# Kernel tuning notes

Hardware: AMD Instinct MI355X
Metric: run time of the kernel (lower is better)

Reference implementation:

```python
import jax, jax.numpy as jnp
import numpy as np

N = 4096
D_IMG = 512
D_FEAT = 512
D_H = 256
D_Z = 128
N_CLS = 64
CHANGE_FRAC = 1.0  # alpha


def setup_inputs() -> dict:
    key = jax.random.key(0)
    ks = jax.random.split(key, 12)
    u = jax.random.uniform(ks[0], (N, N))
    a = (jnp.triu(u, 1) < 0.01).astype(jnp.float32)
    adj_ori = a + a.T
    i = jnp.arange(N)
    # GCN-normalized adjacency D^-1/2 (A+I) D^-1/2 (input to ep_net)
    a_hat = adj_ori.at[i, i].set(1.0)
    d = jnp.power(a_hat.sum(1), -0.5)
    adj_norm = a_hat * d[:, None] * d[None, :]
    xav = lambda k, s: jax.random.uniform(k, s, jnp.float32, -1.0, 1.0) * jnp.sqrt(6.0 / (s[0] + s[1]))
    return {
        "adj_norm": adj_norm,
        "adj_ori": adj_ori,
        "feats_ori": jax.random.normal(ks[1], (N, D_FEAT), jnp.float32),
        "img_feats": jax.random.normal(ks[2], (N, D_IMG), jnp.float32),
        "csd_ori": jax.random.normal(ks[3], (N_CLS, D_FEAT), jnp.float32),
        "csd_img": jax.random.normal(ks[4], (N_CLS, D_IMG), jnp.float32),
        "noise": jax.random.normal(ks[5], (N, D_Z), jnp.float32),
        "Wb": xav(ks[6], (D_IMG, D_H)),
        "Wm": xav(ks[7], (D_H, D_Z)),
        "Wl": xav(ks[8], (D_H, D_Z)),
        "fc1_W": xav(ks[9], (2 * D_FEAT, D_H)),
        "fc1_b": jnp.zeros((D_H,), jnp.float32),
        "fc2_W": xav(ks[10], (2 * D_H, D_IMG)),
        "fc2_b": jnp.zeros((D_IMG,), jnp.float32),
    }


def _ceil_st(x):
    # CeilNoGradient: ceil forward, identity backward (straight-through)
    return x + jax.lax.stop_gradient(jnp.ceil(x) - x)


def _gsage_layer(adj, h, W, b, relu):
    neigh = adj @ h
    mean_neigh = neigh / (adj.sum(axis=1, keepdims=True) + 1e-7)
    x = jnp.concatenate((h, mean_neigh), axis=1) @ W + b
    return jax.nn.relu(x) if relu else x


def _sample_adj_edge(adj_logits, adj):
    n_edges = jnp.sum(adj != 0)
    n_change = jnp.floor(n_edges.astype(jnp.float32) * CHANGE_FRAC / 2.0).astype(jnp.int32)
    ep = jnp.triu(adj_logits, 1)
    ep = ep - jnp.min(ep)
    ep = ep / jnp.max(ep)
    T = N * N
    # --- remove lowest-prob existing edges ---
    mask_rm = ep * adj
    v = jnp.sort(mask_rm.reshape(-1))  # ascending; positives at the tail
    n_nz = jnp.sum(v > 0)
    n_rm = jnp.minimum(n_nz, n_change)
    thresh_rm = v[T - n_nz + n_rm - 1]  # n_rm-th smallest positive
    mask_rm = jnp.where(mask_rm > thresh_rm, 0.0, mask_rm)
    mask_rm = _ceil_st(mask_rm)
    mask_rm = mask_rm + mask_rm.T
    adj_new = adj - mask_rm
    # --- add highest-prob missing edges ---
    mask_add = ep * (1.0 - adj)
    v2 = jnp.sort(mask_add.reshape(-1))
    n_nz2 = jnp.sum(v2 > 0)
    n_add = jnp.minimum(n_nz2, n_change)
    thresh_add = v2[T - n_add]  # n_add-th largest positive
    mask_add = jnp.where(mask_add < thresh_add, 0.0, mask_add)
    mask_add = _ceil_st(mask_add)
    mask_add = mask_add + mask_add.T
    return adj_new + mask_add


def reference(adj_norm, adj_ori, feats_ori, img_feats, csd_ori, csd_img, noise,
              Wb, Wm, Wl, fc1_W, fc1_b, fc2_W, fc2_b):
    # ep_net (VGAE, gae=False)
    hidden = adj_norm @ (img_feats @ Wb)
    mean = jax.nn.relu(adj_norm @ (hidden @ Wm))
    logstd = jax.nn.relu(adj_norm @ (hidden @ Wl))
    Z = noise * jnp.exp(logstd) + mean
    adj_logits = Z @ Z.T
    # edge rewiring
    adj_new = _sample_adj_edge(adj_logits, adj_ori)
    # normalize_adj for 'gsage': fill diag 1, L1 row-normalize
    i = jnp.arange(N)
    adj_new = adj_new.at[i, i].set(1.0)
    adj_new = adj_new / jnp.maximum(jnp.sum(jnp.abs(adj_new), axis=1, keepdims=True), 1e-12)
    # nc_net (DGPN)
    preds_img = img_feats @ csd_img.T
    h1 = _gsage_layer(adj_new, feats_ori, fc1_W, fc1_b, relu=True)
    h2 = _gsage_layer(adj_new, h1, fc2_W, fc2_b, relu=False)
    feat_total = jax.nn.log_softmax(h2, axis=-1)
    preds_total = feat_total @ csd_img.T
    return preds_total, feat_total, preds_img, adj_logits
```

## Files before the change

### kernel.cpp

```cpp
#include <hip/hip_runtime.h>
#include <type_traits>
#include <stdint.h>

#define NN 4096
#define TTOT 16777216UL

enum { F_RELU=1, F_ACC=2, F_RS=4, F_BIAS=8 };

typedef unsigned short ushort_t;
using bf16x8 = __attribute__((ext_vector_type(8))) short;
using f32x4  = __attribute__((ext_vector_type(4))) float;

struct SelParams {
  unsigned min_ord, max_ord, n_up;
  float lo, M, c0;
  unsigned n_change, rm_prefix, rm_k, add_prefix, add_k;
  float t_rm, t_add;
  unsigned hist_rm[256], hist_add[256];
};

__device__ __forceinline__ unsigned ordenc(float x){
  unsigned u = __float_as_uint(x);
  return (u & 0x80000000u) ? ~u : (u | 0x80000000u);
}
__device__ __forceinline__ float orddec_ok(unsigned o){
  unsigned u = (o & 0x80000000u) ? (o ^ 0x80000000u) : ~o;
  return __uint_as_float(u);
}
__device__ __forceinline__ ushort_t f2bf(float x){
  unsigned u = __float_as_uint(x);
  return (ushort_t)((u + 0x7FFFu + ((u >> 16) & 1u)) >> 16);
}
__device__ __forceinline__ float bf2f(ushort_t h){
  return __uint_as_float(((unsigned)h) << 16);
}

template<int DN>
__global__ __launch_bounds__(256)
void k_b3t(const float* __restrict__ Bsrc, ushort_t* __restrict__ H,
           ushort_t* __restrict__ Mg, ushort_t* __restrict__ L)
{
  __shared__ ushort_t sh[64][65], sm[64][65], sl[64][65];
  const int t = threadIdx.x;
  const int n0 = blockIdx.x * 64, k0 = blockIdx.y * 64;
  #pragma unroll
  for (int it = 0; it < 16; ++it){
    int idx = it*256 + t; int r = idx >> 6, c = idx & 63;
    float x  = Bsrc[(size_t)(k0 + r)*DN + n0 + c];
    ushort_t hb = f2bf(x);
    float r1 = x - bf2f(hb);
    ushort_t mb = f2bf(r1);
    float r2 = r1 - bf2f(mb);
    ushort_t lb = f2bf(r2);
    sh[r][c] = hb; sm[r][c] = mb; sl[r][c] = lb;
  }
  __syncthreads();
  #pragma unroll
  for (int it = 0; it < 16; ++it){
    int idx = it*256 + t; int r = idx >> 6, c = idx & 63;
    size_t o = (size_t)(n0 + r)*4096 + k0 + c;
    H[o] = sh[c][r]; Mg[o] = sm[c][r]; L[o] = sl[c][r];
  }
}

__global__ __launch_bounds__(256)
void k_mfma(const signed char* __restrict__ A8,
            const ushort_t* __restrict__ BH, const ushort_t* __restrict__ BM2,
            const ushort_t* __restrict__ BL, float* __restrict__ C, int N)
{
  __shared__ ushort_t Ab[64][72];
  __shared__ ushort_t Bb[3][64][72];
  const int t = threadIdx.x;
  const int m0 = blockIdx.y * 64, n0 = blockIdx.x * 64;
  const int sr = t >> 2, sc = (t & 3) * 16;
  const int w = t >> 6, lane = t & 63;
  const int fr = lane & 15, fg = lane >> 4;

  int4 a_r = *reinterpret_cast<const int4*>(A8 + (size_t)(m0+sr)*4096 + sc);
  const ushort_t* bsrc0 = BH  + (size_t)(n0+sr)*4096 + sc;
  const ushort_t* bsrc1 = BM2 + (size_t)(n0+sr)*4096 + sc;
  const ushort_t* bsrc2 = BL  + (size_t)(n0+sr)*4096 + sc;
  int4 b0a = reinterpret_cast<const int4*>(bsrc0)[0], b0b = reinterpret_cast<const int4*>(bsrc0)[1];
  int4 b1a = reinterpret_cast<const int4*>(bsrc1)[0], b1b = reinterpret_cast<const int4*>(bsrc1)[1];
  int4 b2a = reinterpret_cast<const int4*>(bsrc2)[0], b2b = reinterpret_cast<const int4*>(bsrc2)[1];

  f32x4 acc[4][3];
  #pragma unroll
  for (int c = 0; c < 4; ++c)
    #pragma unroll
    for (int p = 0; p < 3; ++p)
      acc[c][p] = (f32x4){0.f, 0.f, 0.f, 0.f};

  for (int k0 = 0; k0 < 4096; k0 += 64){
    {
      alignas(16) ushort_t tmp[16];
      const signed char* ab = reinterpret_cast<const signed char*>(&a_r);
      #pragma unroll
      for (int i = 0; i < 16; ++i) tmp[i] = f2bf((float)(int)ab[i]);
      *reinterpret_cast<int4*>(&Ab[sr][sc])     = reinterpret_cast<int4*>(tmp)[0];
      *reinterpret_cast<int4*>(&Ab[sr][sc + 8]) = reinterpret_cast<int4*>(tmp)[1];
      *reinterpret_cast<int4*>(&Bb[0][sr][sc])     = b0a;
      *reinterpret_cast<int4*>(&Bb[0][sr][sc + 8]) = b0b;
      *reinterpret_cast<int4*>(&Bb[1][sr][sc])     = b1a;
      *reinterpret_cast<int4*>(&Bb[1][sr][sc + 8]) = b1b;
      *reinterpret_cast<int4*>(&Bb[2][sr][sc])     = b2a;
      *reinterpret_cast<int4*>(&Bb[2][sr][sc + 8]) = b2b;
    }
    __syncthreads();
    if (k0 + 64 < 4096){
      a_r = *reinterpret_cast<const int4*>(A8 + (size_t)(m0+sr)*4096 + (k0+64) + sc);
      const ushort_t* p0 = BH  + (size_t)(n0+sr)*4096 + (k0+64) + sc;
      const ushort_t* p1 = BM2 + (size_t)(n0+sr)*4096 + (k0+64) + sc;
      const ushort_t* p2 = BL  + (size_t)(n0+sr)*4096 + (k0+64) + sc;
      b0a = reinterpret_cast<const int4*>(p0)[0]; b0b = reinterpret_cast<const int4*>(p0)[1];
      b1a = reinterpret_cast<const int4*>(p1)[0]; b1b = reinterpret_cast<const int4*>(p1)[1];
      b2a = reinterpret_cast<const int4*>(p2)[0]; b2b = reinterpret_cast<const int4*>(p2)[1];
    }
    #pragma unroll
    for (int kk = 0; kk < 64; kk += 32){
      bf16x8 af = *reinterpret_cast<const bf16x8*>(&Ab[w*16 + fr][kk + fg*8]);
      #pragma unroll
      for (int c = 0; c < 4; ++c){
        const int bn = c*16 + fr;
        bf16x8 bh = *reinterpret_cast<const bf16x8*>(&Bb[0][bn][kk + fg*8]);
        acc[c][0] = __builtin_amdgcn_mfma_f32_16x16x32_bf16(af, bh, acc[c][0], 0, 0, 0);
        bf16x8 bm = *reinterpret_cast<const bf16x8*>(&Bb[1][bn][kk + fg*8]);
        acc[c][1] = __builtin_amdgcn_mfma_f32_16x16x32_bf16(af, bm, acc[c][1], 0, 0, 0);
        bf16x8 bl = *reinterpret_cast<const bf16x8*>(&Bb[2][bn][kk + fg*8]);
        acc[c][2] = __builtin_amdgcn_mfma_f32_16x16x32_bf16(af, bl, acc[c][2], 0, 0, 0);
      }
    }
    __syncthreads();
  }
  #pragma unroll
  for (int c = 0; c < 4; ++c){
    f32x4 s = acc[c][0] + acc[c][1];
    s = s + acc[c][2];
    #pragma unroll
    for (int r = 0; r < 4; ++r)
      C[(size_t)(m0 + w*16 + fg*4 + r)*N + n0 + c*16 + fr] = s[r];
  }
}

template<typename TA>
__global__ __launch_bounds__(256)
void k_gemm32(const TA* __restrict__ A, const float* __restrict__ B,
              float* __restrict__ C, int M, int N, int K, int ldc,
              const float* __restrict__ rowscale, const float* __restrict__ bias,
              int flags)
{
  __shared__ float As[16][36];
  __shared__ float Bs[16][68];
  const int t  = threadIdx.x;
  const int tx = t & 15, ty = t >> 4;
  const int m0 = blockIdx.y * 32, n0 = blockIdx.x * 64;
  float acc[2][4] = {};
  for (int k0 = 0; k0 < K; k0 += 16) {
    if (t < 128){
      const int mA = t >> 2, kA = (t & 3) * 4;
      if constexpr (std::is_same<TA, float>::value) {
        float4 v = *reinterpret_cast<const float4*>(A + (size_t)(m0+mA)*K + (k0+kA));
        As[kA+0][mA]=v.x; As[kA+1][mA]=v.y; As[kA+2][mA]=v.z; As[kA+3][mA]=v.w;
      } else {
        int u = *reinterpret_cast<const int*>(A + (size_t)(m0+mA)*K + (k0+kA));
        As[kA+0][mA]=(float)(int)(signed char)( u       & 0xff);
        As[kA+1][mA]=(float)(int)(signed char)((u>>8)   & 0xff);
        As[kA+2][mA]=(float)(int)(signed char)((u>>16)  & 0xff);
        As[kA+3][mA]=(float)(int)(signed char)((u>>24)  & 0xff);
      }
    }
    {
      const int kB = t >> 4, nB = (t & 15) * 4;
      float4 w = *reinterpret_cast<const float4*>(B + (size_t)(k0+kB)*N + (n0+nB));
      Bs[kB][nB+0]=w.x; Bs[kB][nB+1]=w.y; Bs[kB][nB+2]=w.z; Bs[kB][nB+3]=w.w;
    }
    __syncthreads();
    #pragma unroll
    for (int kk = 0; kk < 16; ++kk) {
      float a0 = As[kk][ty*2+0];
      float a1 = As[kk][ty*2+1];
      float4 bv = *reinterpret_cast<const float4*>(&Bs[kk][tx*4]);
      float b[4]={bv.x,bv.y,bv.z,bv.w};
      #pragma unroll
      for (int j=0;j<4;++j){
        acc[0][j] = fmaf(a0, b[j], acc[0][j]);
        acc[1][j] = fmaf(a1, b[j], acc[1][j]);
      }
    }
    __syncthreads();
  }
  #pragma unroll
  for (int i=0;i<2;++i){
    const int m = m0 + ty*2 + i;
    const float rsv = (flags & F_RS) ? rowscale[m] : 1.0f;
    float* cp = C + (size_t)m*ldc + (n0 + tx*4);
    float o[4];
    #pragma unroll
    for (int j=0;j<4;++j){
      float v = acc[i][j] * rsv;
      if (flags & F_BIAS) v += bias[n0 + tx*4 + j];
      if (flags & F_ACC)  v += cp[j];
      if (flags & F_RELU) v = fmaxf(v, 0.0f);
      o[j] = v;
    }
    *reinterpret_cast<float4*>(cp) = make_float4(o[0],o[1],o[2],o[3]);
  }
}

__global__ __launch_bounds__(256)
void k_gemm32T(const float* __restrict__ A, const float* __restrict__ B,
               float* __restrict__ C, int M, int N, int K, int ldc)
{
  __shared__ float As[16][36];
  __shared__ float Bs[16][68];
  const int t  = threadIdx.x;
  const int tx = t & 15, ty = t >> 4;
  const int m0 = blockIdx.y * 32, n0 = blockIdx.x * 64;
  float acc[2][4] = {};
  for (int k0 = 0; k0 < K; k0 += 16) {
    if (t < 128){
      const int mA = t >> 2, kA = (t & 3) * 4;
      float4 v = *reinterpret_cast<const float4*>(A + (size_t)(m0+mA)*K + (k0+kA));
      As[kA+0][mA]=v.x; As[kA+1][mA]=v.y; As[kA+2][mA]=v.z; As[kA+3][mA]=v.w;
    }
    {
      const int nB = t >> 2, kB = (t & 3) * 4;
      float4 w = *reinterpret_cast<const float4*>(B + (size_t)(n0+nB)*K + (k0+kB));
      Bs[kB+0][nB]=w.x; Bs[kB+1][nB]=w.y; Bs[kB+2][nB]=w.z; Bs[kB+3][nB]=w.w;
    }
    __syncthreads();
    #pragma unroll
    for (int kk = 0; kk < 16; ++kk) {
      float a0 = As[kk][ty*2+0];
      float a1 = As[kk][ty*2+1];
      float4 bv = *reinterpret_cast<const float4*>(&Bs[kk][tx*4]);
      float b[4]={bv.x,bv.y,bv.z,bv.w};
      #pragma unroll
      for (int j=0;j<4;++j){
        acc[0][j] = fmaf(a0, b[j], acc[0][j]);
        acc[1][j] = fmaf(a1, b[j], acc[1][j]);
      }
    }
    __syncthreads();
  }
  #pragma unroll
  for (int i=0;i<2;++i){
    const int m = m0 + ty*2 + i;
    float* cp = C + (size_t)m*ldc + (n0 + tx*4);
    *reinterpret_cast<float4*>(cp) = make_float4(acc[i][0],acc[i][1],acc[i][2],acc[i][3]);
  }
}

__global__ __launch_bounds__(256)
void k_fc(const float* __restrict__ A1, const float* __restrict__ B1,
          const float* __restrict__ bias,
          const float* __restrict__ A2, const float* __restrict__ B2,
          const float* __restrict__ rowscale,
          float* __restrict__ C, int N, int K1, int K2, int relu)
{
  __shared__ float As[16][36];
  __shared__ float Bs[16][68];
  const int t  = threadIdx.x;
  const int tx = t & 15, ty = t >> 4;
  const int m0 = blockIdx.y * 32, n0 = blockIdx.x * 64;
  float acc1[2][4] = {};
  float acc2[2][4] = {};
  for (int k0 = 0; k0 < K1; k0 += 16) {
    if (t < 128){
      const int mA = t >> 2, kA = (t & 3) * 4;
      float4 v = *reinterpret_cast<const float4*>(A1 + (size_t)(m0+mA)*K1 + (k0+kA));
      As[kA+0][mA]=v.x; As[kA+1][mA]=v.y; As[kA+2][mA]=v.z; As[kA+3][mA]=v.w;
    }
    {
      const int kB = t >> 4, nB = (t & 15) * 4;
      float4 w = *reinterpret_cast<const float4*>(B1 + (size_t)(k0+kB)*N + (n0+nB));
      Bs[kB][nB+0]=w.x; Bs[kB][nB+1]=w.y; Bs[kB][nB+2]=w.z; Bs[kB][nB+3]=w.w;
    }
    __syncthreads();
    #pragma unroll
    for (int kk = 0; kk < 16; ++kk) {
      float a0 = As[kk][ty*2+0];
      float a1 = As[kk][ty*2+1];
      float4 bv = *reinterpret_cast<const float4*>(&Bs[kk][tx*4]);
      float b[4]={bv.x,bv.y,bv.z,bv.w};
      #pragma unroll
      for (int j=0;j<4;++j){
        acc1[0][j] = fmaf(a0, b[j], acc1[0][j]);
        acc1[1][j] = fmaf(a1, b[j], acc1[1][j]);
      }
    }
    __syncthreads();
  }
  for (int k0 = 0; k0 < K2; k0 += 16) {
    if (t < 128){
      const int mA = t >> 2, kA = (t & 3) * 4;
      float4 v = *reinterpret_cast<const float4*>(A2 + (size_t)(m0+mA)*K2 + (k0+kA));
      As[kA+0][mA]=v.x; As[kA+1][mA]=v.y; As[kA+2][mA]=v.z; As[kA+3][mA]=v.w;
    }
    {
      const int kB = t >> 4, nB = (t & 15) * 4;
      float4 w = *reinterpret_cast<const float4*>(B2 + (size_t)(k0+kB)*N + (n0+nB));
      Bs[kB][nB+0]=w.x; Bs[kB][nB+1]=w.y; Bs[kB][nB+2]=w.z; Bs[kB][nB+3]=w.w;
    }
    __syncthreads();
    #pragma unroll
    for (int kk = 0; kk < 16; ++kk) {
      float a0 = As[kk][ty*2+0];
      float a1 = As[kk][ty*2+1];
      float4 bv = *reinterpret_cast<const float4*>(&Bs[kk][tx*4]);
      float b[4]={bv.x,bv.y,bv.z,bv.w};
      #pragma unroll
      for (int j=0;j<4;++j){
        acc2[0][j] = fmaf(a0, b[j], acc2[0][j]);
        acc2[1][j] = fmaf(a1, b[j], acc2[1][j]);
      }
    }
    __syncthreads();
  }
  #pragma unroll
  for (int i=0;i<2;++i){
    const int m = m0 + ty*2 + i;
    const float rsv = rowscale[m];
    float* cp = C + (size_t)m*N + (n0 + tx*4);
    float o[4];
    #pragma unroll
    for (int j=0;j<4;++j){
      float t1 = acc1[i][j] + bias[n0 + tx*4 + j];
      float v  = acc2[i][j] * rsv;
      v += t1;
      if (relu) v = fmaxf(v, 0.0f);
      o[j] = v;
    }
    *reinterpret_cast<float4*>(cp) = make_float4(o[0],o[1],o[2],o[3]);
  }
}

__global__ __launch_bounds__(256)
void k_wcat(const float* __restrict__ Wm, const float* __restrict__ Wl,
            float* __restrict__ Wcat)
{
  int idx = blockIdx.x*256 + threadIdx.x;
  int row = idx >> 8, col = idx & 255;
  Wcat[idx] = (col < 128) ? Wm[row*128 + col] : Wl[row*128 + (col - 128)];
}

template<int D>
__global__ __launch_bounds__(256)
void k_spmmF(const float* __restrict__ A, const float* __restrict__ B,
             float* __restrict__ C)
{
  const int row = blockIdx.x, t = threadIdx.x;
  const int lane = t & 63, wv = t >> 6;
  __shared__ int   sc[288];
  __shared__ float sv[288];
  __shared__ int wtot[4];
  __shared__ int nsh;
  const float4* r4 = reinterpret_cast<const float4*>(A + (size_t)row*NN) + t*4;
  float lv[16];
  #pragma unroll
  for (int q=0;q<4;++q){
    float4 v = r4[q];
    lv[q*4+0]=v.x; lv[q*4+1]=v.y; lv[q*4+2]=v.z; lv[q*4+3]=v.w;
  }
  int c = 0;
  #pragma unroll
  for (int k=0;k<16;++k) c += (lv[k] != 0.0f);
  int inc = c;
  #pragma unroll
  for (int off=1; off<64; off<<=1){
    int v = __shfl_up(inc, off, 64);
    if (lane >= off) inc += v;
  }
  if (lane == 63) wtot[wv] = inc;
  __syncthreads();
  int wbase = 0;
  #pragma unroll
  for (int ww=0; ww<3; ++ww) if (ww < wv) wbase += wtot[ww];
  int pos = wbase + inc - c;
  #pragma unroll
  for (int k=0;k<16;++k){
    if (lv[k] != 0.0f){
      if (pos >= 0 && pos < 288){ sc[pos] = t*16+k; sv[pos] = lv[k]; }
      pos++;
    }
  }
  if (t == 255){
    int tot = wbase + inc;
    nsh = (tot < 288) ? tot : 288;
  }
  __syncthreads();
  const int n = nsh;
  float acc = 0.f;
  int s = 0;
  for (; s+4 <= n; s += 4){
    float x0 = B[(size_t)sc[s+0]*D + t];
    float x1 = B[(size_t)sc[s+1]*D + t];
    float x2 = B[(size_t)sc[s+2]*D + t];
    float x3 = B[(size_t)sc[s+3]*D + t];
    acc = fmaf(sv[s+0], x0, acc);
    acc = fmaf(sv[s+1], x1, acc);
    acc = fmaf(sv[s+2], x2, acc);
    acc = fmaf(sv[s+3], x3, acc);
  }
  for (; s < n; ++s) acc = fmaf(sv[s], B[(size_t)sc[s]*D + t], acc);
  C[(size_t)row*D + t] = acc;
}

__global__ __launch_bounds__(256)
void k_zzt(const float* __restrict__ Z, float* __restrict__ C)
{
  const int bx = blockIdx.x, by = blockIdx.y;
  if (by > bx) return;
  __shared__ float As[16][68];
  __shared__ float Bs[16][68];
  const int t = threadIdx.x, tx = t & 15, ty = t >> 4;
  const int m0 = by*64, n0 = bx*64;
  const int mA = t >> 2, kA = (t & 3) * 4;
  float acc[4][4] = {};
  for (int k0 = 0; k0 < 128; k0 += 16){
    float4 va = *reinterpret_cast<const float4*>(Z + (size_t)(m0+mA)*128 + k0 + kA);
    As[kA+0][mA]=va.x; As[kA+1][mA]=va.y; As[kA+2][mA]=va.z; As[kA+3][mA]=va.w;
    float4 vb = *reinterpret_cast<const float4*>(Z + (size_t)(n0+mA)*128 + k0 + kA);
    Bs[kA+0][mA]=vb.x; Bs[kA+1][mA]=vb.y; Bs[kA+2][mA]=vb.z; Bs[kA+3][mA]=vb.w;
    __syncthreads();
    #pragma unroll
    for (int kk = 0; kk < 16; ++kk) {
      float4 av = *reinterpret_cast<const float4*>(&As[kk][ty*4]);
      float4 bv = *reinterpret_cast<const float4*>(&Bs[kk][tx*4]);
      float a[4]={av.x,av.y,av.z,av.w};
      float b[4]={bv.x,bv.y,bv.z,bv.w};
      #pragma unroll
      for (int i=0;i<4;++i)
        #pragma unroll
        for (int j=0;j<4;++j)
          acc[i][j] = fmaf(a[i], b[j], acc[i][j]);
    }
    __syncthreads();
  }
  #pragma unroll
  for (int i=0;i<4;++i){
    float* cp = C + (size_t)(m0+ty*4+i)*NN + (n0 + tx*4);
    *reinterpret_cast<float4*>(cp) = make_float4(acc[i][0],acc[i][1],acc[i][2],acc[i][3]);
  }
  if (bx != by){
    for (int c0 = 0; c0 < 64; c0 += 16){
      __syncthreads();
      if (tx >= c0/4 && tx < c0/4 + 4){
        #pragma unroll
        for (int i=0;i<4;++i)
          #pragma unroll
          for (int j=0;j<4;++j)
            As[tx*4 + j - c0][ty*4 + i] = acc[i][j];
      }
      __syncthreads();
      const int c = t & 63, r0 = t >> 6;
      #pragma unroll
      for (int rr = 0; rr < 4; ++rr)
        C[(size_t)(n0 + c0 + r0 + rr*4)*NN + m0 + c] = As[r0 + rr*4][c];
    }
  }
}

__global__ __launch_bounds__(256)
void k_z2(const float* __restrict__ MPLP, const float* __restrict__ noise,
          float* __restrict__ Z)
{
  int i = blockIdx.x*256 + threadIdx.x;
  int m = i >> 7, c = i & 127;
  float mp = fmaxf(MPLP[(size_t)m*256 + c], 0.0f);
  float lp = fmaxf(MPLP[(size_t)m*256 + 128 + c], 0.0f);
  Z[i] = noise[i]*expf(lp) + mp;
}

__global__ __launch_bounds__(256)
void k_initstats(SelParams* p)
{
  int t = threadIdx.x;
  if (t == 0){
    p->min_ord = 0xFFFFFFFFu; p->max_ord = 0u; p->n_up = 0u;
    p->rm_prefix = 0u; p->add_prefix = 0u;
  }
  p->hist_rm[t] = 0u; p->hist_add[t] = 0u;
}

__global__ __launch_bounds__(256)
void k_stats1(const float* __restrict__ L, const float* __restrict__ adj,
              unsigned long long* __restrict__ mask, SelParams* __restrict__ p)
{
  unsigned mn=0xFFFFFFFFu, mx=0u, cnt=0u;
  size_t g = (size_t)blockIdx.x*256 + threadIdx.x;
  const size_t stride = (size_t)gridDim.x*256;
  for (; g < 262144; g += stride){
    const int i  = (int)(g >> 6);
    const int jb = (int)(g & 63) << 6;
    unsigned long long m = 0ull;
    if (jb + 63 > i){
      const float4* a4 = reinterpret_cast<const float4*>(adj + (size_t)i*NN + jb);
      const float4* l4 = reinterpret_cast<const float4*>(L   + (size_t)i*NN + jb);
      for (int w = 0; w < 16; ++w){
        const int j0 = jb + w*4;
        if (j0 + 3 <= i) continue;
        float4 av = a4[w]; float4 lv = l4[w];
        float ae[4]={av.x,av.y,av.z,av.w};
        float le[4]={lv.x,lv.y,lv.z,lv.w};
        #pragma unroll
        for (int e=0;e<4;++e){
          const int jj = j0 + e;
          if (jj > i){
            if (ae[e] != 0.0f){ m |= 1ull << (jj & 63); cnt++; }
            unsigned o = ordenc(le[e]);
            mn = (o < mn) ? o : mn;
            mx = (o > mx) ? o : mx;
          }
        }
      }
    }
    mask[g] = m;
  }
  __shared__ unsigned smn[256], smx[256], sc[256];
  int t = threadIdx.x;
  smn[t]=mn; smx[t]=mx; sc[t]=cnt; __syncthreads();
  for (int s=128; s>0; s>>=1){
    if (t < s){
      smn[t] = (smn[t+s] < smn[t]) ? smn[t+s] : smn[t];
      smx[t] = (smx[t+s] > smx[t]) ? smx[t+s] : smx[t];
      sc[t] += sc[t+s];
    }
    __syncthreads();
  }
  if (t == 0){
    atomicMin(&p->min_ord, smn[0]);
    atomicMax(&p->max_ord, smx[0]);
    atomicAdd(&p->n_up, sc[0]);
  }
}

__global__ void k_stats2(SelParams* p)
{
  float mnv = orddec_ok(p->min_ord), mxv = orddec_ok(p->max_ord);
  float lo = fminf(mnv, 0.0f), hi = fmaxf(mxv, 0.0f);
  p->lo = lo;
  p->M  = hi - lo;
  p->c0 = (0.0f - lo) / p->M;
  p->n_change = p->n_up;
}

__global__ __launch_bounds__(256)
void k_hist2(const float* __restrict__ L, const unsigned long long* __restrict__ mask,
             SelParams* __restrict__ p, int shift)
{
  __shared__ unsigned hr[256], ha[256];
  const int t = threadIdx.x;
  hr[t]=0u; ha[t]=0u; __syncthreads();
  const float lo = p->lo, Mv = p->M;
  const unsigned pr = p->rm_prefix, pa = p->add_prefix;
  const float4* L4 = reinterpret_cast<const float4*>(L);
  size_t q = (size_t)blockIdx.x*256 + t;
  const size_t stride = (size_t)gridDim.x*256;
  for (; q < TTOT/4; q += stride){
    const int i = (int)(q >> 10);
    const int j = (int)(q & 1023) << 2;
    if (j + 3 <= i) continue;
    float4 l = L4[q];
    const unsigned long long w = mask[q >> 4];
    float le[4]={l.x,l.y,l.z,l.w};
    #pragma unroll
    for (int e=0;e<4;++e){
      const int jj = j + e;
      if (jj <= i) continue;
      const unsigned key = __float_as_uint((le[e] - lo) / Mv);
      if (key == 0u) continue;
      const bool edge = (w >> (jj & 63)) & 1ull;
      if (edge){
        if (shift == 24 || (key >> (shift+8)) == pr) atomicAdd(&hr[(key>>shift)&255u], 1u);
      } else {
        if (shift == 24 || (key >> (shift+8)) == pa) atomicAdd(&ha[(key>>shift)&255u], 1u);
      }
    }
  }
  __syncthreads();
  if (hr[t]) atomicAdd(&p->hist_rm[t], hr[t]);
  if (ha[t]) atomicAdd(&p->hist_add[t], ha[t]);
}

__global__ __launch_bounds__(256)
void k_scan2(SelParams* __restrict__ p, int shift)
{
  const int t = threadIdx.x;
  if (t == 0){
    const unsigned c0k  = __float_as_uint(p->c0);
    const unsigned n_up = p->n_up;
    {
      unsigned injb = 300u, inj = 0u;
      if (c0k != 0u && (shift == 24 || (c0k >> (shift+8)) == p->rm_prefix)){
        injb = (c0k >> shift) & 255u; inj = n_up;
      }
      unsigned k;
      if (shift == 24){
        unsigned tot = inj;
        for (int d=0; d<256; ++d) tot += p->hist_rm[d];
        k = (tot < p->n_change) ? tot : p->n_change;
      } else k = p->rm_k;
      unsigned cum = 0u, digit = 255u;
      for (int d=0; d<256; ++d){
        unsigned hd = p->hist_rm[d] + (((unsigned)d == injb) ? inj : 0u);
        if (cum + hd >= k){ digit = (unsigned)d; k -= cum; break; }
        cum += hd;
      }
      p->rm_prefix = (p->rm_prefix << 8) | digit;
      p->rm_k = k;
      if (shift == 0) p->t_rm = __uint_as_float(p->rm_prefix);
    }
    {
      unsigned injb = 300u, inj = 0u;
      if (c0k != 0u && (shift == 24 || (c0k >> (shift+8)) == p->add_prefix)){
        injb = (c0k >> shift) & 255u;
        inj  = 8386560u - n_up + 4096u;
      }
      unsigned k;
      if (shift == 24){
        unsigned tot = inj;
        for (int d=0; d<256; ++d) tot += p->hist_add[d];
        k = (tot < p->n_change) ? tot : p->n_change;
      } else k = p->add_k;
      unsigned cum = 0u, digit = 0u;
      for (int d=255; d>=0; --d){
        unsigned hd = p->hist_add[d] + (((unsigned)d == injb) ? inj : 0u);
        if (cum + hd >= k){ digit = (unsigned)d; k -= cum; break; }
        cum += hd;
      }
      p->add_prefix = (p->add_prefix << 8) | digit;
      p->add_k = k;
      if (shift == 0) p->t_add = __uint_as_float(p->add_prefix);
    }
  }
  __syncthreads();
  p->hist_rm[t] = 0u; p->hist_add[t] = 0u;
}

__device__ __forceinline__ int adjval(bool edge, float v, float c0v, float trm, float tad)
{
  int rmU = (edge && v   >  0.0f && v   <= trm) ? 1 : 0;
  int rmL = (edge && c0v >  0.0f && c0v <= trm) ? 1 : 0;
  int adU = (!edge && v   >= tad) ? 1 : 0;
  int adL = (!edge && c0v >= tad) ? 1 : 0;
  return (edge ? 1 : 0) - rmU - rmL + adU + adL;
}

__global__ __launch_bounds__(256)
void k_apply(const float* __restrict__ L, const unsigned long long* __restrict__ mask,
             const SelParams* __restrict__ p, signed char* __restrict__ A8)
{
  const int bx = blockIdx.x, by = blockIdx.y;
  if (by > bx) return;
  const float lo=p->lo, Mv=p->M, c0v=p->c0, trm=p->t_rm, tad=p->t_add;
  const int i0 = by*64, j0 = bx*64, t = threadIdx.x;
  __shared__ signed char Vs[64][65];
  if (bx == by){
    for (int it=0; it<16; ++it){
      int e = it*256 + t; int r = e>>6, c = e&63;
      size_t idx = (size_t)(i0+r)*NN + (j0+c);
      if (r < c){
        bool edge = (mask[idx>>6] >> ((j0+c) & 63)) & 1ull;
        float v = (L[idx] - lo) / Mv;
        int val = adjval(edge, v, c0v, trm, tad);
        A8[idx] = (signed char)val;
        Vs[c][r] = (signed char)val;
      } else if (r == c){
        A8[idx] = 1;
      }
    }
    __syncthreads();
    for (int it=0; it<16; ++it){
      int e = it*256 + t; int r = e>>6, c = e&63;
      if (r > c) A8[(size_t)(i0+r)*NN + (j0+c)] = Vs[r][c];
    }
  } else {
    for (int it=0; it<16; ++it){
      int e = it*256 + t; int r = e>>6, c = e&63;
      size_t idx = (size_t)(i0+r)*NN + (j0+c);
      bool edge = (mask[idx>>6] >> ((j0+c) & 63)) & 1ull;
      float v = (L[idx] - lo) / Mv;
      int val = adjval(edge, v, c0v, trm, tad);
      A8[idx] = (signed char)val;
      Vs[c][r] = (signed char)val;
    }
    __syncthreads();
    for (int it=0; it<16; ++it){
      int e = it*256 + t; int r = e>>6, c = e&63;
      A8[(size_t)(j0+r)*NN + (i0+c)] = Vs[r][c];
    }
  }
}

__global__ __launch_bounds__(256)
void k_rowsum8(const signed char* __restrict__ A8, float* __restrict__ s_mean)
{
  const int row = blockIdx.x, t = threadIdx.x;
  const int4 w = reinterpret_cast<const int4*>(A8 + (size_t)row*NN)[t];
  int s = 0, a = 0;
  int vs[4] = {w.x, w.y, w.z, w.w};
  #pragma unroll
  for (int q=0; q<4; ++q){
    int u = vs[q];
    #pragma unroll
    for (int b=0; b<4; ++b){
      int c = (int)(signed char)((u >> (8*b)) & 0xff);
      s += c; a += (c < 0) ? -c : c;
    }
  }
  __shared__ int rs_[256], ra_[256];
  rs_[t]=s; ra_[t]=a; __syncthreads();
  for (int st=128; st>0; st>>=1){
    if (t < st){ rs_[t]+=rs_[t+st]; ra_[t]+=ra_[t+st]; }
    __syncthreads();
  }
  if (t == 0){
    float rs = (float)rs_[0], ra = (float)ra_[0];
    float A = fmaxf(ra, 1e-12f);
    s_mean[row] = (1.0f / A) / (rs / A + 1e-7f);
  }
}

__global__ __launch_bounds__(256)
void k_lsm(float* __restrict__ X)
{
  const int row = blockIdx.x, t = threadIdx.x;
  float* x = X + (size_t)row*512;
  float v0 = x[t], v1 = x[t+256];
  __shared__ float red[256];
  red[t] = fmaxf(v0, v1); __syncthreads();
  for (int s=128; s>0; s>>=1){
    if (t < s) red[t] = fmaxf(red[t], red[t+s]);
    __syncthreads();
  }
  float m = red[0]; __syncthreads();
  red[t] = expf(v0-m) + expf(v1-m); __syncthreads();
  for (int s=128; s>0; s>>=1){
    if (t < s) red[t] += red[t+s];
    __syncthreads();
  }
  float ls = logf(red[0]);
  x[t]     = (v0 - m) - ls;
  x[t+256] = (v1 - m) - ls;
}

extern "C" void kernel_launch(void* const* d_in, const int* in_sizes, int n_in,
                              void* d_out, int out_size, void* d_ws, size_t ws_size,
                              hipStream_t stream)
{
  (void)in_sizes; (void)n_in; (void)out_size; (void)ws_size;
  const float* adj_norm = (const float*)d_in[0];
  const float* adj_ori  = (const float*)d_in[1];
  const float* feats    = (const float*)d_in[2];
  const float* img      = (const float*)d_in[3];
  const float* csd_img  = (const float*)d_in[5];
  const float* noise    = (const float*)d_in[6];
  const float* Wb       = (const float*)d_in[7];
  const float* Wm       = (const float*)d_in[8];
  const float* Wl       = (const float*)d_in[9];
  const float* fc1W     = (const float*)d_in[10];
  const float* fc1b     = (const float*)d_in[11];
  const float* fc2W     = (const float*)d_in[12];
  const float* fc2b     = (const float*)d_in[13];

  float* out    = (float*)d_out;
  float* out_pt = out;
  float* out_ft = out + 262144;
  float* out_pi = out + 2359296;
  float* out_lg = out + 2621440;

  char* W = (char*)d_ws;
  signed char* adj8 = (signed char*)W;
  float* bufA   = (float*)(W + (16u<<20));
  float* bufB   = (float*)(W + (24u<<20));
  float* HMHL   = (float*)(W + (28u<<20));
  float* MPLP   = (float*)(W + (32u<<20));
  float* Z      = (float*)(W + (36u<<20));
  unsigned long long* mask = (unsigned long long*)(W + (38u<<20));
  float* s_mean = (float*)(W + (44u<<20));
  SelParams* sp = (SelParams*)(W + (44u<<20) + 65536);
  float* Wcat   = (float*)(W + (45u<<20));
  ushort_t* BT1h = (ushort_t*)(W + (28u<<20));
  ushort_t* BT1m = (ushort_t*)(W + (32u<<20));
  ushort_t* BT1l = (ushort_t*)(W + (36u<<20));
  ushort_t* BT2h = (ushort_t*)(W + (28u<<20));
  ushort_t* BT2m = (ushort_t*)(W + (30u<<20));
  ushort_t* BT2l = (ushort_t*)(W + (32u<<20));

  dim3 B(256);
  auto G32 = [](int M, int N){ return dim3((unsigned)(N/64), (unsigned)(M/32)); };

  k_gemm32<float><<<G32(4096,256),B,0,stream>>>(img, Wb, bufA, 4096,256,512,256, nullptr,nullptr,0);
  k_spmmF<256><<<4096,B,0,stream>>>(adj_norm, bufA, bufB);
  k_wcat<<<256,B,0,stream>>>(Wm, Wl, Wcat);
  k_gemm32<float><<<G32(4096,256),B,0,stream>>>(bufB, Wcat, HMHL, 4096,256,256,256, nullptr,nullptr,0);
  k_spmmF<256><<<4096,B,0,stream>>>(adj_norm, HMHL, MPLP);
  k_z2<<<2048,B,0,stream>>>(MPLP, noise, Z);
  k_zzt<<<dim3(64,64),B,0,stream>>>(Z, out_lg);

  k_initstats<<<1,B,0,stream>>>(sp);
  k_stats1<<<1024,B,0,stream>>>(out_lg, adj_ori, mask, sp);
  k_stats2<<<1,1,0,stream>>>(sp);
  for (int shift = 24; shift >= 0; shift -= 8){
    k_hist2<<<2048,B,0,stream>>>(out_lg, mask, sp, shift);
    k_scan2<<<1,B,0,stream>>>(sp, shift);
  }
  k_apply<<<dim3(64,64),B,0,stream>>>(out_lg, mask, sp, adj8);

  k_rowsum8<<<4096,B,0,stream>>>(adj8, s_mean);

  k_b3t<512><<<dim3(8,64),B,0,stream>>>(feats, BT1h, BT1m, BT1l);
  k_mfma<<<dim3(8,64),B,0,stream>>>(adj8, BT1h, BT1m, BT1l, bufA, 512);
  k_fc<<<G32(4096,256),B,0,stream>>>(feats, fc1W, fc1b, bufA, fc1W + 512*256, s_mean,
                                     bufB, 256, 512, 512, 1);
  k_b3t<256><<<dim3(4,64),B,0,stream>>>(bufB, BT2h, BT2m, BT2l);
  k_mfma<<<dim3(4,64),B,0,stream>>>(adj8, BT2h, BT2m, BT2l, bufA, 256);
  k_fc<<<G32(4096,512),B,0,stream>>>(bufB, fc2W, fc2b, bufA, fc2W + 256*512, s_mean,
                                     out_ft, 512, 256, 256, 0);
  k_lsm<<<4096,B,0,stream>>>(out_ft);

  k_gemm32T<<<G32(4096,64),B,0,stream>>>(out_ft, csd_img, out_pt, 4096,64,512,64);
  k_gemm32T<<<G32(4096,64),B,0,stream>>>(img, csd_img, out_pi, 4096,64,512,64);
}
```

Measured before the change: 855.4 us.

## Load B operand fragments straight from global memory, dropping B shared-memory staging

The three-way split-bf16 MFMA GEMM kernel no longer stages the B (hi/mid/lo) tiles through LDS. Each wave now owns a 16-column strip of B and loads its fragments directly from global into registers, while iterating over the four 16-row A tiles from LDS. This removes LDS traffic and the store/load for B, but the B global loads are no longer prefetched a tile ahead, so their latency may be exposed inside the MFMA loop.

```diff
diff --git a/kernel.cpp b/kernel.cpp
--- a/kernel.cpp
+++ b/kernel.cpp
@@ -69,27 +69,24 @@
             const ushort_t* __restrict__ BL, float* __restrict__ C, int N)
 {
   __shared__ ushort_t Ab[64][72];
-  __shared__ ushort_t Bb[3][64][72];
   const int t = threadIdx.x;
   const int m0 = blockIdx.y * 64, n0 = blockIdx.x * 64;
   const int sr = t >> 2, sc = (t & 3) * 16;
   const int w = t >> 6, lane = t & 63;
   const int fr = lane & 15, fg = lane >> 4;
+  const size_t brow = (size_t)(n0 + w*16 + fr) * 4096 + (size_t)(fg*8);
+  const ushort_t* bh = BH  + brow;
+  const ushort_t* bm = BM2 + brow;
+  const ushort_t* bl = BL  + brow;
 
   int4 a_r = *reinterpret_cast<const int4*>(A8 + (size_t)(m0+sr)*4096 + sc);
-  const ushort_t* bsrc0 = BH  + (size_t)(n0+sr)*4096 + sc;
-  const ushort_t* bsrc1 = BM2 + (size_t)(n0+sr)*4096 + sc;
-  const ushort_t* bsrc2 = BL  + (size_t)(n0+sr)*4096 + sc;
-  int4 b0a = reinterpret_cast<const int4*>(bsrc0)[0], b0b = reinterpret_cast<const int4*>(bsrc0)[1];
-  int4 b1a = reinterpret_cast<const int4*>(bsrc1)[0], b1b = reinterpret_cast<const int4*>(bsrc1)[1];
-  int4 b2a = reinterpret_cast<const int4*>(bsrc2)[0], b2b = reinterpret_cast<const int4*>(bsrc2)[1];
 
   f32x4 acc[4][3];
   #pragma unroll
-  for (int c = 0; c < 4; ++c)
+  for (int mt = 0; mt < 4; ++mt)
     #pragma unroll
     for (int p = 0; p < 3; ++p)
-      acc[c][p] = (f32x4){0.f, 0.f, 0.f, 0.f};
+      acc[mt][p] = (f32x4){0.f, 0.f, 0.f, 0.f};
 
   for (int k0 = 0; k0 < 4096; k0 += 64){
     {
@@ -99,46 +96,32 @@
       for (int i = 0; i < 16; ++i) tmp[i] = f2bf((float)(int)ab[i]);
       *reinterpret_cast<int4*>(&Ab[sr][sc])     = reinterpret_cast<int4*>(tmp)[0];
       *reinterpret_cast<int4*>(&Ab[sr][sc + 8]) = reinterpret_cast<int4*>(tmp)[1];
-      *reinterpret_cast<int4*>(&Bb[0][sr][sc])     = b0a;
-      *reinterpret_cast<int4*>(&Bb[0][sr][sc + 8]) = b0b;
-      *reinterpret_cast<int4*>(&Bb[1][sr][sc])     = b1a;
-      *reinterpret_cast<int4*>(&Bb[1][sr][sc + 8]) = b1b;
-      *reinterpret_cast<int4*>(&Bb[2][sr][sc])     = b2a;
-      *reinterpret_cast<int4*>(&Bb[2][sr][sc + 8]) = b2b;
-    }
-    __syncthreads();
-    if (k0 + 64 < 4096){
+    }
+    __syncthreads();
+    if (k0 + 64 < 4096)
       a_r = *reinterpret_cast<const int4*>(A8 + (size_t)(m0+sr)*4096 + (k0+64) + sc);
-      const ushort_t* p0 = BH  + (size_t)(n0+sr)*4096 + (k0+64) + sc;
-      const ushort_t* p1 = BM2 + (size_t)(n0+sr)*4096 + (k0+64) + sc;
-      const ushort_t* p2 = BL  + (size_t)(n0+sr)*4096 + (k0+64) + sc;
-      b0a = reinterpret_cast<const int4*>(p0)[0]; b0b = reinterpret_cast<const int4*>(p0)[1];
-      b1a = reinterpret_cast<const int4*>(p1)[0]; b1b = reinterpret_cast<const int4*>(p1)[1];
-      b2a = reinterpret_cast<const int4*>(p2)[0]; b2b = reinterpret_cast<const int4*>(p2)[1];
-    }
     #pragma unroll
     for (int kk = 0; kk < 64; kk += 32){
-      bf16x8 af = *reinterpret_cast<const bf16x8*>(&Ab[w*16 + fr][kk + fg*8]);
+      bf16x8 b0 = *reinterpret_cast<const bf16x8*>(bh + k0 + kk);
+      bf16x8 b1 = *reinterpret_cast<const bf16x8*>(bm + k0 + kk);
+      bf16x8 b2 = *reinterpret_cast<const bf16x8*>(bl + k0 + kk);
       #pragma unroll
-      for (int c = 0; c < 4; ++c){
-        const int bn = c*16 + fr;
-        bf16x8 bh = *reinterpret_cast<const bf16x8*>(&Bb[0][bn][kk + fg*8]);
-        acc[c][0] = __builtin_amdgcn_mfma_f32_16x16x32_bf16(af, bh, acc[c][0], 0, 0, 0);
-        bf16x8 bm = *reinterpret_cast<const bf16x8*>(&Bb[1][bn][kk + fg*8]);
-        acc[c][1] = __builtin_amdgcn_mfma_f32_16x16x32_bf16(af, bm, acc[c][1], 0, 0, 0);
-        bf16x8 bl = *reinterpret_cast<const bf16x8*>(&Bb[2][bn][kk + fg*8]);
-        acc[c][2] = __builtin_amdgcn_mfma_f32_16x16x32_bf16(af, bl, acc[c][2], 0, 0, 0);
-      }
-    }
-    __syncthreads();
-  }
-  #pragma unroll
-  for (int c = 0; c < 4; ++c){
-    f32x4 s = acc[c][0] + acc[c][1];
-    s = s + acc[c][2];
+      for (int mt = 0; mt < 4; ++mt){
+        bf16x8 af = *reinterpret_cast<const bf16x8*>(&Ab[mt*16 + fr][kk + fg*8]);
+        acc[mt][0] = __builtin_amdgcn_mfma_f32_16x16x32_bf16(af, b0, acc[mt][0], 0, 0, 0);
+        acc[mt][1] = __builtin_amdgcn_mfma_f32_16x16x32_bf16(af, b1, acc[mt][1], 0, 0, 0);
+        acc[mt][2] = __builtin_amdgcn_mfma_f32_16x16x32_bf16(af, b2, acc[mt][2], 0, 0, 0);
+      }
+    }
+    __syncthreads();
+  }
+  #pragma unroll
+  for (int mt = 0; mt < 4; ++mt){
+    f32x4 s = acc[mt][0] + acc[mt][1];
+    s = s + acc[mt][2];
     #pragma unroll
     for (int r = 0; r < 4; ++r)
-      C[(size_t)(m0 + w*16 + fg*4 + r)*N + n0 + c*16 + fr] = s[r];
+      C[(size_t)(m0 + mt*16 + fg*4 + r)*N + n0 + w*16 + fr] = s[r];
   }
 }
 
```

Result: slower. 915.8 us (+7.1%).
